# Kernel tuning notes

Measured on AMD Instinct MI355X. Metric: run time of the kernel, lower is better.

Reference implementation:

```python
import jax, jax.numpy as jnp
import numpy as np

EPS = 1e-5
QB = 127.0  # int8 activation quantization bound

def rmsnorm(x):
    # SimpleRMSNorm: x / rms(x), no learned scale
    return x * jax.lax.rsqrt(jnp.mean(x * x, axis=-1, keepdims=True) + EPS)

def activation_quant(x):
    # per-token absmax int8 quant-dequant
    scale = QB / jnp.clip(jnp.max(jnp.abs(x), axis=-1, keepdims=True), EPS)
    return jnp.clip(jnp.round(x * scale), -QB - 1, QB) / scale

def weight_quant(w):
    # per-tensor ternary quant-dequant (BitNet b1.58)
    scale = 1.0 / jnp.clip(jnp.mean(jnp.abs(w)), EPS)
    return jnp.clip(jnp.round(w * scale), -1.0, 1.0) / scale

def ste(x, q):
    # straight-through estimator: forward uses q, gradient flows to x
    return x + jax.lax.stop_gradient(q - x)

def bitlinear(x, w, b):
    xn = rmsnorm(x)
    xq = ste(xn, activation_quant(xn))
    wq = ste(w, weight_quant(w))
    # x: [b, s, d_in], w: [d_out, d_in] -> [b, s, d_out]
    return jnp.einsum('bsd,od->bso', xq, wq) + b

def setup_inputs() -> dict:
    key = jax.random.key(0)
    k1, k2, k3, k4, k5 = jax.random.split(key, 5)
    dim, inner = 1024, 4096
    x = jax.random.normal(k1, (4, 4096, dim), dtype=jnp.float32)
    w1 = jax.random.normal(k2, (inner, dim), dtype=jnp.float32) * (dim ** -0.5)
    b1 = jax.random.normal(k3, (inner,), dtype=jnp.float32) * 0.02
    w2 = jax.random.normal(k4, (dim, inner), dtype=jnp.float32) * (inner ** -0.5)
    b2 = jax.random.normal(k5, (dim,), dtype=jnp.float32) * 0.02
    return {"x": x, "w1": w1, "b1": b1, "w2": w2, "b2": b2}

def reference(x, w1, b1, w2, b2):
    h = jax.nn.gelu(bitlinear(x, w1, b1), approximate=False)  # torch nn.GELU default = exact erf
    # dropout p=0.0 is identity; post_act_ln disabled
    return bitlinear(h, w2, b2)
```

## Files before the change

### kernel.cpp

```cpp
#include <hip/hip_runtime.h>

#define TOK   16384
#define DIM   1024
#define INNER 4096
#define EPSF  1e-5f

typedef int v4i  __attribute__((ext_vector_type(4)));
typedef int v16i __attribute__((ext_vector_type(16)));

static __device__ __forceinline__ void async_copy16(const char* g, char* l) {
    __builtin_amdgcn_global_load_lds(
        (const __attribute__((address_space(1))) unsigned int*)g,
        (__attribute__((address_space(3))) unsigned int*)l, 16, 0, 0);
}

static __device__ __forceinline__ float bf2f(unsigned short u) {
    return __uint_as_float(((unsigned)u) << 16);
}
static __device__ __forceinline__ unsigned short f2bf(float f) {
    unsigned u = __float_as_uint(f);
    return (unsigned short)((u + 0x7fffu + ((u >> 16) & 1u)) >> 16);
}

static __device__ __forceinline__ float fast_erf(float z) {
    float az = fabsf(z);
    float tt = __builtin_amdgcn_rcpf(1.f + 0.3275911f * az);
    float poly = ((((1.061405429f * tt - 1.453152027f) * tt + 1.421413741f) * tt
                   - 0.284496736f) * tt + 0.254829592f) * tt;
    float er = 1.f - poly * __expf(-az * az);
    return copysignf(er, z);
}
static __device__ __forceinline__ float gelu_exact(float v) {
    return 0.5f * v * (1.f + fast_erf(v * 0.70710678118654752f));
}

static __device__ __forceinline__ float waveSum(float v) {
#pragma unroll
    for (int o = 32; o > 0; o >>= 1) v += __shfl_down(v, o, 64);
    return v;
}
static __device__ __forceinline__ float waveMax(float v) {
#pragma unroll
    for (int o = 32; o > 0; o >>= 1) v = fmaxf(v, __shfl_down(v, o, 64));
    return v;
}

__global__ void absmean_k(const float* __restrict__ w, int n4, float* __restrict__ acc) {
    int idx = blockIdx.x * blockDim.x + threadIdx.x;
    int stride = gridDim.x * blockDim.x;
    const float4* w4 = (const float4*)w;
    float s = 0.f;
    for (int i = idx; i < n4; i += stride) {
        float4 v = w4[i];
        s += fabsf(v.x) + fabsf(v.y) + fabsf(v.z) + fabsf(v.w);
    }
    __shared__ float sp[4];
    int wv = threadIdx.x >> 6, lane = threadIdx.x & 63;
    s = waveSum(s);
    if (lane == 0) sp[wv] = s;
    __syncthreads();
    if (threadIdx.x == 0) atomicAdd(acc, sp[0] + sp[1] + sp[2] + sp[3]);
}

__global__ void wquant_k(const float* __restrict__ w, int n,
                         const float* __restrict__ acc, float* __restrict__ wscale,
                         char* __restrict__ wq) {
    float mean = *acc / (float)n;
    float cl = fmaxf(mean, EPSF);
    float s = 1.f / cl;
    if (blockIdx.x == 0 && threadIdx.x == 0) *wscale = cl;
    int idx = blockIdx.x * blockDim.x + threadIdx.x;
    int stride = gridDim.x * blockDim.x;
    int n4 = n >> 2;
    const float4* w4 = (const float4*)w;
    unsigned* q4 = (unsigned*)wq;
    for (int i = idx; i < n4; i += stride) {
        float4 v = w4[i];
        float e[4] = {v.x, v.y, v.z, v.w};
        unsigned packed = 0;
#pragma unroll
        for (int j = 0; j < 4; j++) {
            float r = rintf(e[j] * s);
            r = fminf(fmaxf(r, -1.f), 1.f);
            packed |= ((unsigned)((int)r & 0xff)) << (8 * j);
        }
        q4[i] = packed;
    }
}

template <int D, int VPT>
__global__ void actquant_f32_k(const float* __restrict__ X, char* __restrict__ Q,
                               float* __restrict__ rs_out) {
    int token = blockIdx.x;
    int t = threadIdx.x;
    const float4* xp = (const float4*)(X + (long)token * D);
    float vals[VPT];
    float ss = 0.f, am = 0.f;
#pragma unroll
    for (int j = 0; j < VPT / 4; j++) {
        float4 v = xp[t * (VPT / 4) + j];
        vals[4 * j] = v.x; vals[4 * j + 1] = v.y; vals[4 * j + 2] = v.z; vals[4 * j + 3] = v.w;
        ss += v.x * v.x + v.y * v.y + v.z * v.z + v.w * v.w;
        am = fmaxf(am, fmaxf(fmaxf(fabsf(v.x), fabsf(v.y)), fmaxf(fabsf(v.z), fabsf(v.w))));
    }
    __shared__ float sp[8];
    __shared__ float bc[2];
    int wv = t >> 6, lane = t & 63;
    float S = waveSum(ss);
    float M = waveMax(am);
    if (lane == 0) { sp[wv] = S; sp[4 + wv] = M; }
    __syncthreads();
    if (t == 0) {
        float Sa = sp[0] + sp[1] + sp[2] + sp[3];
        float Ma = fmaxf(fmaxf(sp[4], sp[5]), fmaxf(sp[6], sp[7]));
        float rinv = rsqrtf(Sa * (1.f / (float)D) + EPSF);
        float amn = Ma * rinv;
        float scale = 127.f / fmaxf(amn, EPSF);
        rs_out[token] = 1.f / scale;
        bc[0] = rinv; bc[1] = scale;
    }
    __syncthreads();
    float rinv = bc[0], scale = bc[1];
    unsigned outw[VPT / 4];
#pragma unroll
    for (int j = 0; j < VPT; j++) {
        float r = rintf((vals[j] * rinv) * scale);
        r = fminf(fmaxf(r, -128.f), 127.f);
        unsigned qi = (unsigned)((int)r & 0xff) << (8 * (j & 3));
        if ((j & 3) == 0) outw[j / 4] = qi; else outw[j / 4] |= qi;
    }
    unsigned* qp = (unsigned*)(Q + (long)token * D);
#pragma unroll
    for (int j = 0; j < VPT / 4; j++) qp[t * (VPT / 4) + j] = outw[j];
}

template <int D, int VPT>
__global__ void actquant_bf16_k(const unsigned short* __restrict__ X, char* __restrict__ Q,
                                float* __restrict__ rs_out) {
    int token = blockIdx.x;
    int t = threadIdx.x;
    const uint4* xp = (const uint4*)(X + (long)token * D);
    float vals[VPT];
    float ss = 0.f, am = 0.f;
#pragma unroll
    for (int j = 0; j < VPT / 8; j++) {
        uint4 v = xp[t * (VPT / 8) + j];
        unsigned ws[4] = {v.x, v.y, v.z, v.w};
#pragma unroll
        for (int p = 0; p < 4; p++) {
            float f0 = gelu_exact(bf2f((unsigned short)(ws[p] & 0xffff)));
            float f1 = gelu_exact(bf2f((unsigned short)(ws[p] >> 16)));
            vals[8 * j + 2 * p] = f0; vals[8 * j + 2 * p + 1] = f1;
            ss += f0 * f0 + f1 * f1;
            am = fmaxf(am, fmaxf(fabsf(f0), fabsf(f1)));
        }
    }
    __shared__ float sp[8];
    __shared__ float bc[2];
    int wv = t >> 6, lane = t & 63;
    float S = waveSum(ss);
    float M = waveMax(am);
    if (lane == 0) { sp[wv] = S; sp[4 + wv] = M; }
    __syncthreads();
    if (t == 0) {
        float Sa = sp[0] + sp[1] + sp[2] + sp[3];
        float Ma = fmaxf(fmaxf(sp[4], sp[5]), fmaxf(sp[6], sp[7]));
        float rinv = rsqrtf(Sa * (1.f / (float)D) + EPSF);
        float amn = Ma * rinv;
        float scale = 127.f / fmaxf(amn, EPSF);
        rs_out[token] = 1.f / scale;
        bc[0] = rinv; bc[1] = scale;
    }
    __syncthreads();
    float rinv = bc[0], scale = bc[1];
    unsigned outw[4];
#pragma unroll
    for (int j = 0; j < VPT; j++) {
        float r = rintf((vals[j] * rinv) * scale);
        r = fminf(fmaxf(r, -128.f), 127.f);
        unsigned qi = (unsigned)((int)r & 0xff) << (8 * (j & 3));
        if ((j & 3) == 0) outw[j / 4] = qi; else outw[j / 4] |= qi;
    }
    uint4* qp = (uint4*)(Q + (long)token * D);
    qp[t] = make_uint4(outw[0], outw[1], outw[2], outw[3]);
}

template <int OUT_F32>
__global__ __launch_bounds__(512, 2) void gemm8_k(
    const char* __restrict__ A, const char* __restrict__ Bw,
    const float* __restrict__ rs, const float* __restrict__ wscale_p,
    const float* __restrict__ bias, void* __restrict__ outp,
    int M, int N, int K) {
    __shared__ char L[131072];
    int t = threadIdx.x;
    int lane = t & 63, wv = t >> 6;
    int l31 = lane & 31, kh = lane >> 5;
    int wmi = wv >> 2, wni = wv & 3;
    int m0 = blockIdx.y * 256, n0 = blockIdx.x * 256;

    const char* srcA0 = A  + (long)(m0 + (t & 255)) * K + ((t >> 8) * 16);
    const char* srcB0 = Bw + (long)(n0 + (t & 255)) * K + ((t >> 8) * 16);
    char* dA = L + (size_t)t * 16;
    char* dB = L + 32768 + (size_t)t * 16;

    auto stA = [&](int Tt, int kb) {
        const char* g = srcA0 + ((long)Tt << 7) + kb * 64;
        char* l = dA + (Tt & 1) * 65536 + kb * 16384;
        async_copy16(g, l);
        async_copy16(g + 32, l + 8192);
    };
    auto stB = [&](int Tt, int kb) {
        const char* g = srcB0 + ((long)Tt << 7) + kb * 64;
        char* l = dB + (Tt & 1) * 65536 + kb * 16384;
        async_copy16(g, l);
        async_copy16(g + 32, l + 8192);
    };

    const char* rdA = L + kh * 4096 + (size_t)(wmi * 128 + l31) * 16;
    const char* rdB = L + 32768 + kh * 4096 + (size_t)(wni * 64 + l31) * 16;

    v16i acc[4][2] = {};
    int nK = K >> 7;

    stA(0, 0); stB(0, 0); stA(0, 1); stB(0, 1);
    asm volatile("s_waitcnt vmcnt(4)" ::: "memory");
    __builtin_amdgcn_s_barrier();

    for (int T = 0; T < nK; ++T) {
        int bo = (T & 1) * 65536;
        bool pre = (T + 1 < nK);
#pragma unroll
        for (int ks = 0; ks < 4; ++ks) {
            const char* pa = rdA + bo + ks * 8192;
            const char* pb = rdB + bo + ks * 8192;
            v4i a0 = *(const v4i*)(pa);
            v4i a1 = *(const v4i*)(pa + 512);
            v4i a2 = *(const v4i*)(pa + 1024);
            v4i a3 = *(const v4i*)(pa + 1536);
            v4i b0 = *(const v4i*)(pb);
            v4i b1 = *(const v4i*)(pb + 512);
            if (pre) {
                if (ks == 0) stA(T + 1, 0);
                else if (ks == 1) stB(T + 1, 0);
                else if (ks == 2) stA(T + 1, 1);
                else stB(T + 1, 1);
            }
            __builtin_amdgcn_s_barrier();
            __builtin_amdgcn_s_setprio(1);
            acc[0][0] = __builtin_amdgcn_mfma_i32_32x32x32_i8(a0, b0, acc[0][0], 0, 0, 0);
            acc[0][1] = __builtin_amdgcn_mfma_i32_32x32x32_i8(a0, b1, acc[0][1], 0, 0, 0);
            acc[1][0] = __builtin_amdgcn_mfma_i32_32x32x32_i8(a1, b0, acc[1][0], 0, 0, 0);
            acc[1][1] = __builtin_amdgcn_mfma_i32_32x32x32_i8(a1, b1, acc[1][1], 0, 0, 0);
            acc[2][0] = __builtin_amdgcn_mfma_i32_32x32x32_i8(a2, b0, acc[2][0], 0, 0, 0);
            acc[2][1] = __builtin_amdgcn_mfma_i32_32x32x32_i8(a2, b1, acc[2][1], 0, 0, 0);
            acc[3][0] = __builtin_amdgcn_mfma_i32_32x32x32_i8(a3, b0, acc[3][0], 0, 0, 0);
            acc[3][1] = __builtin_amdgcn_mfma_i32_32x32x32_i8(a3, b1, acc[3][1], 0, 0, 0);
            __builtin_amdgcn_s_setprio(0);
            if (ks == 1) {
                if (pre) asm volatile("s_waitcnt vmcnt(4)" ::: "memory");
                else     asm volatile("s_waitcnt vmcnt(0)" ::: "memory");
            }
            if (ks == 3 && pre) asm volatile("s_waitcnt vmcnt(4)" ::: "memory");
            __builtin_amdgcn_s_barrier();
        }
    }

    float wsc = *wscale_p;
    float bv[2];
#pragma unroll
    for (int j = 0; j < 2; j++) bv[j] = bias[n0 + wni * 64 + j * 32 + l31];
#pragma unroll
    for (int i = 0; i < 4; i++) {
        int mbase = m0 + wmi * 128 + i * 32 + 4 * kh;
        float fsv[16];
#pragma unroll
        for (int rg = 0; rg < 16; rg++)
            fsv[rg] = rs[mbase + (rg & 3) + 8 * (rg >> 2)] * wsc;
#pragma unroll
        for (int j = 0; j < 2; j++) {
            int ng = n0 + wni * 64 + j * 32 + l31;
#pragma unroll
            for (int rg = 0; rg < 16; rg++) {
                int mg = mbase + (rg & 3) + 8 * (rg >> 2);
                float v = (float)acc[i][j][rg] * fsv[rg] + bv[j];
                long idx = (long)mg * N + ng;
                if (OUT_F32) ((float*)outp)[idx] = v;
                else ((unsigned short*)outp)[idx] = f2bf(v);
            }
        }
    }
}

extern "C" void kernel_launch(void* const* d_in, const int* in_sizes, int n_in,
                              void* d_out, int out_size, void* d_ws, size_t ws_size,
                              hipStream_t stream) {
    const float* x  = (const float*)d_in[0];
    const float* w1 = (const float*)d_in[1];
    const float* b1 = (const float*)d_in[2];
    const float* w2 = (const float*)d_in[3];
    const float* b2 = (const float*)d_in[4];
    float* out = (float*)d_out;

    char* ws = (char*)d_ws;
    float* acc1 = (float*)(ws + 0);
    float* acc2 = (float*)(ws + 4);
    float* wsc1 = (float*)(ws + 8);
    float* wsc2 = (float*)(ws + 12);
    size_t off = 256;
    char* w1q = ws + off; off += (size_t)INNER * DIM;
    char* w2q = ws + off; off += (size_t)INNER * DIM;
    char* xq1 = ws + off; off += (size_t)TOK * DIM;
    float* rs1 = (float*)(ws + off); off += (size_t)TOK * 4;
    char* xq2 = ws + off; off += (size_t)TOK * INNER;
    float* rs2 = (float*)(ws + off); off += (size_t)TOK * 4;
    unsigned short* h = (unsigned short*)(ws + off);

    hipMemsetAsync(d_ws, 0, 16, stream);

    int nw = INNER * DIM;
    absmean_k<<<1024, 256, 0, stream>>>(w1, nw / 4, acc1);
    absmean_k<<<1024, 256, 0, stream>>>(w2, nw / 4, acc2);
    wquant_k<<<2048, 256, 0, stream>>>(w1, nw, acc1, wsc1, w1q);
    wquant_k<<<2048, 256, 0, stream>>>(w2, nw, acc2, wsc2, w2q);

    actquant_f32_k<DIM, 4><<<TOK, 256, 0, stream>>>(x, xq1, rs1);
    gemm8_k<0><<<dim3(INNER / 256, TOK / 256), 512, 0, stream>>>(
        xq1, w1q, rs1, wsc1, b1, (void*)h, TOK, INNER, DIM);
    actquant_bf16_k<INNER, 16><<<TOK, 256, 0, stream>>>(h, xq2, rs2);
    gemm8_k<1><<<dim3(DIM / 256, TOK / 256), 512, 0, stream>>>(
        xq2, w2q, rs2, wsc2, b2, (void*)out, TOK, DIM, INNER);
}
```

Before: 439.2 us.

## Replace 256x256 int8 GEMM with 256x128 four-wave kernel and grid swizzle

The int8 MFMA GEMM changes from a 512-thread, 256x256 tile with a 128-deep K step and 128KB LDS to a 256-thread, 256x128 tile with a 64-deep K step and 48KB of LDS. It also adds an XCD-style block-index swizzle and a simpler double-buffer schedule: one vmcnt(0) wait and one barrier per K tile, replacing the per-substep barriers. The smaller LDS footprint and fewer barriers aim at higher occupancy and less synchronisation stall. In exchange, per-block reuse drops, so more global traffic per FLOP, and the wait-all per tile exposes load latency more directly.

```diff
diff --git a/kernel.cpp b/kernel.cpp
--- a/kernel.cpp
+++ b/kernel.cpp
@@ -186,66 +186,73 @@
 }
 
 template <int OUT_F32>
-__global__ __launch_bounds__(512, 2) void gemm8_k(
+__global__ __launch_bounds__(256, 2) void gemm4_k(
     const char* __restrict__ A, const char* __restrict__ Bw,
     const float* __restrict__ rs, const float* __restrict__ wscale_p,
     const float* __restrict__ bias, void* __restrict__ outp,
     int M, int N, int K) {
-    __shared__ char L[131072];
+    __shared__ char L[49152];
     int t = threadIdx.x;
     int lane = t & 63, wv = t >> 6;
     int l31 = lane & 31, kh = lane >> 5;
-    int wmi = wv >> 2, wni = wv & 3;
-    int m0 = blockIdx.y * 256, n0 = blockIdx.x * 256;
-
-    const char* srcA0 = A  + (long)(m0 + (t & 255)) * K + ((t >> 8) * 16);
-    const char* srcB0 = Bw + (long)(n0 + (t & 255)) * K + ((t >> 8) * 16);
-    char* dA = L + (size_t)t * 16;
-    char* dB = L + 32768 + (size_t)t * 16;
-
-    auto stA = [&](int Tt, int kb) {
-        const char* g = srcA0 + ((long)Tt << 7) + kb * 64;
-        char* l = dA + (Tt & 1) * 65536 + kb * 16384;
-        async_copy16(g, l);
-        async_copy16(g + 32, l + 8192);
+    int wmi = wv >> 1, wni = wv & 1;
+
+    int gx = gridDim.x;
+    int nwg = gx * gridDim.y;
+    int bid = blockIdx.y * gx + blockIdx.x;
+    int swz = (bid & 7) * (nwg >> 3) + (bid >> 3);
+    int bx = swz % gx, by = swz / gx;
+    int m0 = by * 256, n0 = bx * 128;
+
+    const char* srcA = A  + (long)(m0 + wv * 16 + (lane & 15)) * K + ((lane >> 4) * 16);
+    const char* srcB = Bw + (long)(n0 + wv * 16 + (lane & 15)) * K + ((lane >> 4) * 16);
+    char* dstA = L + wv * 1024 + lane * 16;
+    char* dstB = L + 32768 + wv * 1024 + lane * 16;
+
+    auto stA = [&](int Tt, int q) {
+        async_copy16(srcA + (long)q * 64 * K + ((long)Tt << 6),
+                     dstA + (Tt & 1) * 16384 + q * 4096);
     };
-    auto stB = [&](int Tt, int kb) {
-        const char* g = srcB0 + ((long)Tt << 7) + kb * 64;
-        char* l = dB + (Tt & 1) * 65536 + kb * 16384;
-        async_copy16(g, l);
-        async_copy16(g + 32, l + 8192);
+    auto stB = [&](int Tt, int q) {
+        async_copy16(srcB + (long)q * 64 * K + ((long)Tt << 6),
+                     dstB + (Tt & 1) * 8192 + q * 4096);
     };
 
-    const char* rdA = L + kh * 4096 + (size_t)(wmi * 128 + l31) * 16;
-    const char* rdB = L + 32768 + kh * 4096 + (size_t)(wni * 64 + l31) * 16;
+    int offA[4], offB[2];
+#pragma unroll
+    for (int i = 0; i < 4; i++) {
+        int r = wmi * 128 + i * 32 + l31;
+        offA[i] = (r >> 4) * 1024 + (r & 15) * 16 + kh * 256;
+    }
+#pragma unroll
+    for (int j = 0; j < 2; j++) {
+        int r = wni * 64 + j * 32 + l31;
+        offB[j] = (r >> 4) * 1024 + (r & 15) * 16 + kh * 256;
+    }
 
     v16i acc[4][2] = {};
-    int nK = K >> 7;
-
-    stA(0, 0); stB(0, 0); stA(0, 1); stB(0, 1);
-    asm volatile("s_waitcnt vmcnt(4)" ::: "memory");
-    __builtin_amdgcn_s_barrier();
+    int nK = K >> 6;
+
+    stA(0, 0); stA(0, 1); stA(0, 2); stA(0, 3); stB(0, 0); stB(0, 1);
+    asm volatile("s_waitcnt vmcnt(0)" ::: "memory");
+    asm volatile("s_barrier" ::: "memory");
 
     for (int T = 0; T < nK; ++T) {
-        int bo = (T & 1) * 65536;
+        const char* pA = L + (T & 1) * 16384;
+        const char* pB = L + 32768 + (T & 1) * 8192;
         bool pre = (T + 1 < nK);
 #pragma unroll
-        for (int ks = 0; ks < 4; ++ks) {
-            const char* pa = rdA + bo + ks * 8192;
-            const char* pb = rdB + bo + ks * 8192;
-            v4i a0 = *(const v4i*)(pa);
-            v4i a1 = *(const v4i*)(pa + 512);
-            v4i a2 = *(const v4i*)(pa + 1024);
-            v4i a3 = *(const v4i*)(pa + 1536);
-            v4i b0 = *(const v4i*)(pb);
-            v4i b1 = *(const v4i*)(pb + 512);
+        for (int ks = 0; ks < 2; ++ks) {
+            v4i a0 = *(const v4i*)(pA + offA[0] + ks * 512);
+            v4i a1 = *(const v4i*)(pA + offA[1] + ks * 512);
+            v4i a2 = *(const v4i*)(pA + offA[2] + ks * 512);
+            v4i a3 = *(const v4i*)(pA + offA[3] + ks * 512);
+            v4i b0 = *(const v4i*)(pB + offB[0] + ks * 512);
+            v4i b1 = *(const v4i*)(pB + offB[1] + ks * 512);
             if (pre) {
-                if (ks == 0) stA(T + 1, 0);
-                else if (ks == 1) stB(T + 1, 0);
-                else if (ks == 2) stA(T + 1, 1);
-                else stB(T + 1, 1);
+                if (ks == 0) { stA(T + 1, 0); stA(T + 1, 1); stB(T + 1, 0); }
+                else         { stA(T + 1, 2); stA(T + 1, 3); stB(T + 1, 1); }
             }
-            __builtin_amdgcn_s_barrier();
             __builtin_amdgcn_s_setprio(1);
             acc[0][0] = __builtin_amdgcn_mfma_i32_32x32x32_i8(a0, b0, acc[0][0], 0, 0, 0);
             acc[0][1] = __builtin_amdgcn_mfma_i32_32x32x32_i8(a0, b1, acc[0][1], 0, 0, 0);
@@ -256,13 +263,9 @@
             acc[3][0] = __builtin_amdgcn_mfma_i32_32x32x32_i8(a3, b0, acc[3][0], 0, 0, 0);
             acc[3][1] = __builtin_amdgcn_mfma_i32_32x32x32_i8(a3, b1, acc[3][1], 0, 0, 0);
             __builtin_amdgcn_s_setprio(0);
-            if (ks == 1) {
-                if (pre) asm volatile("s_waitcnt vmcnt(4)" ::: "memory");
-                else     asm volatile("s_waitcnt vmcnt(0)" ::: "memory");
-            }
-            if (ks == 3 && pre) asm volatile("s_waitcnt vmcnt(4)" ::: "memory");
-            __builtin_amdgcn_s_barrier();
         }
+        asm volatile("s_waitcnt vmcnt(0)" ::: "memory");
+        asm volatile("s_barrier" ::: "memory");
     }
 
     float wsc = *wscale_p;
@@ -324,9 +327,9 @@
     wquant_k<<<2048, 256, 0, stream>>>(w2, nw, acc2, wsc2, w2q);
 
     actquant_f32_k<DIM, 4><<<TOK, 256, 0, stream>>>(x, xq1, rs1);
-    gemm8_k<0><<<dim3(INNER / 256, TOK / 256), 512, 0, stream>>>(
+    gemm4_k<0><<<dim3(INNER / 128, TOK / 256), 256, 0, stream>>>(
         xq1, w1q, rs1, wsc1, b1, (void*)h, TOK, INNER, DIM);
     actquant_bf16_k<INNER, 16><<<TOK, 256, 0, stream>>>(h, xq2, rs2);
-    gemm8_k<1><<<dim3(DIM / 256, TOK / 256), 512, 0, stream>>>(
+    gemm4_k<1><<<dim3(DIM / 128, TOK / 256), 256, 0, stream>>>(
         xq2, w2q, rs2, wsc2, b2, (void*)out, TOK, DIM, INNER);
 }
```

Result: no change. 438.6 us (-0.1%).
